# Kernel tuning notes

Measured on AMD Instinct MI355X. Metric: run time of the kernel, lower is better.

## Reference

```python
import jax, jax.numpy as jnp
import numpy as np

B, N, D_IN, D_HID, D_OUT = 4096, 64, 128, 128, 128


def setup_inputs() -> dict:
    key = jax.random.key(0)
    k1, k2, k3, k4, k5, k6 = jax.random.split(key, 6)
    inp = jax.random.normal(k1, (B, D_IN), dtype=jnp.float32)
    neigh = jax.random.normal(k2, (B, N, D_IN), dtype=jnp.float32)
    # zero out some neighbors so the mask path is exercised
    drop = jax.random.bernoulli(k3, 0.2, (B, N))
    neigh = jnp.where(drop[:, :, None], 0.0, neigh)
    W_mlp = jax.random.normal(k4, (D_HID, D_IN), dtype=jnp.float32) * (1.0 / np.sqrt(D_IN))
    b_mlp = jnp.zeros((D_HID,), dtype=jnp.float32)
    W_comb = jax.random.normal(k5, (2 * D_OUT, D_IN + D_HID), dtype=jnp.float32) * (1.0 / np.sqrt(D_IN + D_HID))
    b_comb = jax.random.normal(k6, (2 * D_OUT,), dtype=jnp.float32) * 0.01
    return {"input": inp, "neighbor_inputs": neigh, "W_mlp": W_mlp, "b_mlp": b_mlp,
            "W_comb": W_comb, "b_comb": b_comb}


def reference(input, neighbor_inputs, W_mlp, b_mlp, W_comb, b_comb):
    # mask: neighbors whose features sum to exactly 0 (padding)  [B, N, 1]
    mask = (jnp.sum(neighbor_inputs, axis=-1) == 0.0)[:, :, None]
    # per-neighbor MLP + ReLU: [B, N, D_HID]
    h = jax.nn.relu(jnp.einsum('bnd,hd->bnh', neighbor_inputs, W_mlp) + b_mlp)
    h = jnp.where(mask, 0.0, h)
    # max-pool over neighbor dim -> [B, D_HID]
    pooled = jnp.max(h, axis=1)
    # combine: concat + linear + ReLU -> [B, 2*D_OUT]
    combined = jnp.concatenate([input, pooled], axis=-1)
    out = jax.nn.relu(combined @ W_comb.T + b_comb)
    return out
```

## Files before the change

### kernel.cpp

```cpp
#include <hip/hip_runtime.h>
#include <hip/hip_bf16.h>

typedef __attribute__((ext_vector_type(4))) float f32x4;
typedef __attribute__((ext_vector_type(8))) short bf16x8;

#define N_NEI 64
#define D_IN  128
#define D_HID 128

union BF8 { bf16x8 v; __hip_bfloat162 h[4]; unsigned u[4]; };

__device__ __forceinline__ bf16x8 pack8(const float4& a, const float4& b) {
  BF8 r;
  r.h[0] = __float22bfloat162_rn(float2{a.x, a.y});
  r.h[1] = __float22bfloat162_rn(float2{a.z, a.w});
  r.h[2] = __float22bfloat162_rn(float2{b.x, b.y});
  r.h[3] = __float22bfloat162_rn(float2{b.z, b.w});
  return r.v;
}

__global__ __launch_bounds__(256, 4)
void k1_pool(const float* __restrict__ neigh, const float* __restrict__ Wmlp,
             const float* __restrict__ bmlp, unsigned short* __restrict__ pooled) {
  __shared__ unsigned short Wl[D_HID * D_IN];
  __shared__ float pscr[4][D_HID];

  const int tid = threadIdx.x;
  const int l = tid & 63;
  const int w = tid >> 6;
  const int lr = l & 15;
  const int lg = l >> 4;

  const int b = blockIdx.x * 4 + w;
  const float* rowbase = neigh + (size_t)b * N_NEI * D_IN;

  float4 pf[8];
  {
    const float* arow = rowbase + (size_t)lr * D_IN + lg * 8;
    #pragma unroll
    for (int ks = 0; ks < 4; ++ks) {
      pf[2 * ks]     = *(const float4*)(arow + ks * 32);
      pf[2 * ks + 1] = *(const float4*)(arow + ks * 32 + 4);
    }
  }

  const float4* W4 = (const float4*)Wmlp;
  #pragma unroll 4
  for (int it = 0; it < 8; ++it) {
    int f8 = it * 256 + tid;
    int j  = f8 >> 4;
    int d0 = (f8 & 15) * 8;
    float4 a = W4[f8 * 2];
    float4 bb = W4[f8 * 2 + 1];
    int byte = j * 256 + ((d0 * 2) ^ ((j & 7) << 4));
    *(bf16x8*)((char*)Wl + byte) = pack8(a, bb);
  }

  float bml[8];
  #pragma unroll
  for (int t = 0; t < 8; ++t) bml[t] = bmlp[t * 16 + lr];

  __syncthreads();

  float pmax[8];
  #pragma unroll
  for (int t = 0; t < 8; ++t) pmax[t] = 0.f;

  #pragma unroll 1
  for (int mt = 0; mt < 4; ++mt) {
    bf16x8 af[4];
    float rs = 0.f;
    #pragma unroll
    for (int ks = 0; ks < 4; ++ks) {
      float4 a0 = pf[2 * ks];
      float4 a1 = pf[2 * ks + 1];
      rs += a0.x + a0.y + a0.z + a0.w + a1.x + a1.y + a1.z + a1.w;
      af[ks] = pack8(a0, a1);
    }

    if (mt < 3) {
      const float* arow = rowbase + (size_t)((mt + 1) * 16 + lr) * D_IN + lg * 8;
      #pragma unroll
      for (int ks = 0; ks < 4; ++ks) {
        pf[2 * ks]     = *(const float4*)(arow + ks * 32);
        pf[2 * ks + 1] = *(const float4*)(arow + ks * 32 + 4);
      }
    }

    rs += __shfl_xor(rs, 16);
    rs += __shfl_xor(rs, 32);
    unsigned mask16 = (unsigned)(__ballot(rs == 0.0f) & 0xFFFFull);

    #pragma unroll 1
    for (int p = 0; p < 2; ++p) {
      f32x4 acc[4];
      #pragma unroll
      for (int tt = 0; tt < 4; ++tt) acc[tt] = (f32x4){0.f, 0.f, 0.f, 0.f};

      #pragma unroll
      for (int tt = 0; tt < 4; ++tt) {
        #pragma unroll
        for (int ks = 0; ks < 4; ++ks) {
          int jr = (p * 4 + tt) * 16 + lr;
          int d0 = ks * 32 + lg * 8;
          bf16x8 bf = *(const bf16x8*)((const char*)Wl + jr * 256 + ((d0 * 2) ^ ((jr & 7) << 4)));
          acc[tt] = __builtin_amdgcn_mfma_f32_16x16x32_bf16(af[ks], bf, acc[tt], 0, 0, 0);
        }
      }

      #pragma unroll
      for (int tt = 0; tt < 4; ++tt) {
        #pragma unroll
        for (int r = 0; r < 4; ++r) {
          int row = lg * 4 + r;
          float v = fmaxf(acc[tt][r] + bml[p * 4 + tt], 0.f);
          if ((mask16 >> row) & 1u) v = 0.f;
          pmax[p * 4 + tt] = fmaxf(pmax[p * 4 + tt], v);
        }
      }
    }
  }

  #pragma unroll
  for (int t = 0; t < 8; ++t) {
    pmax[t] = fmaxf(pmax[t], __shfl_xor(pmax[t], 16));
    pmax[t] = fmaxf(pmax[t], __shfl_xor(pmax[t], 32));
  }

  if (l < 16) {
    #pragma unroll
    for (int t = 0; t < 8; ++t) pscr[w][t * 16 + l] = pmax[t];
  }
  __syncthreads();
  float2 pv = *(const float2*)&pscr[w][2 * l];
  __hip_bfloat162 h2 = __float22bfloat162_rn(pv);
  ((unsigned*)(pooled + (size_t)b * D_HID))[l] = *(unsigned*)&h2;
}

__global__ __launch_bounds__(256, 2)
void k2_comb(const float* __restrict__ inp, const unsigned short* __restrict__ pooled,
             const float* __restrict__ Wcomb, const float* __restrict__ bcomb,
             float* __restrict__ out) {
  __shared__ unsigned short Wl[32 * 256];

  const int tid = threadIdx.x;
  const int l = tid & 63;
  const int w = tid >> 6;
  const int mchunk = blockIdx.x >> 3;
  const int c8     = blockIdx.x & 7;
  const int lr = l & 15;
  const int lg = l >> 4;

  const int row = mchunk * 64 + w * 16 + lr;

  float4 a0[4], a1[4];
  #pragma unroll
  for (int ks = 0; ks < 4; ++ks) {
    const float* p = inp + (size_t)row * 128 + ks * 32 + lg * 8;
    a0[ks] = *(const float4*)p;
    a1[ks] = *(const float4*)(p + 4);
  }
  bf16x8 af[8];
  #pragma unroll
  for (int ks = 4; ks < 8; ++ks) {
    af[ks] = *(const bf16x8*)(pooled + (size_t)row * 128 + (ks - 4) * 32 + lg * 8);
  }

  const float4* W4 = (const float4*)Wcomb;
  #pragma unroll
  for (int it = 0; it < 4; ++it) {
    int c  = it * 256 + tid;
    int jr = c >> 5;
    int d0 = (c & 31) * 8;
    int gidx = ((c8 * 32 + jr) * 256 + d0) >> 2;
    float4 a = W4[gidx];
    float4 bb = W4[gidx + 1];
    int byte = jr * 512 + ((d0 * 2) ^ ((jr & 7) << 4));
    *(bf16x8*)((char*)Wl + byte) = pack8(a, bb);
  }

  float bcl[2];
  #pragma unroll
  for (int t = 0; t < 2; ++t) bcl[t] = bcomb[c8 * 32 + t * 16 + lr];

  #pragma unroll
  for (int ks = 0; ks < 4; ++ks) af[ks] = pack8(a0[ks], a1[ks]);

  __syncthreads();

  f32x4 acc[2];
  #pragma unroll
  for (int t = 0; t < 2; ++t) acc[t] = (f32x4){0.f, 0.f, 0.f, 0.f};
  #pragma unroll
  for (int t = 0; t < 2; ++t) {
    #pragma unroll
    for (int ks = 0; ks < 8; ++ks) {
      int jr = t * 16 + lr;
      int d0 = ks * 32 + lg * 8;
      bf16x8 bf = *(const bf16x8*)((const char*)Wl + jr * 512 + ((d0 * 2) ^ ((jr & 7) << 4)));
      acc[t] = __builtin_amdgcn_mfma_f32_16x16x32_bf16(af[ks], bf, acc[t], 0, 0, 0);
    }
  }

  #pragma unroll
  for (int t = 0; t < 2; ++t) {
    #pragma unroll
    for (int r = 0; r < 4; ++r) {
      int ro = mchunk * 64 + w * 16 + lg * 4 + r;
      int co = c8 * 32 + t * 16 + lr;
      float v = acc[t][r] + bcl[t];
      out[(size_t)ro * 256 + co] = fmaxf(v, 0.f);
    }
  }
}

extern "C" void kernel_launch(void* const* d_in, const int* in_sizes, int n_in,
                              void* d_out, int out_size, void* d_ws, size_t ws_size,
                              hipStream_t stream) {
  const float* inp   = (const float*)d_in[0];
  const float* neigh = (const float*)d_in[1];
  const float* Wmlp  = (const float*)d_in[2];
  const float* bmlp  = (const float*)d_in[3];
  const float* Wcomb = (const float*)d_in[4];
  const float* bcomb = (const float*)d_in[5];
  float* out = (float*)d_out;
  unsigned short* pooled = (unsigned short*)d_ws;

  k1_pool<<<1024, 256, 0, stream>>>(neigh, Wmlp, bmlp, pooled);
  k2_comb<<<512, 256, 0, stream>>>(inp, pooled, Wcomb, bcomb, out);
}
```

Baseline: 42.92 us.

## Fuse neighbor max-pool and combine linear into a single kernel

```diff
diff --git a/kernel.cpp b/kernel.cpp
--- a/kernel.cpp
+++ b/kernel.cpp
@@ -19,11 +19,13 @@
   return r.v;
 }
 
-__global__ __launch_bounds__(256, 4)
-void k1_pool(const float* __restrict__ neigh, const float* __restrict__ Wmlp,
-             const float* __restrict__ bmlp, unsigned short* __restrict__ pooled) {
+__global__ __launch_bounds__(256, 2)
+void fused_pool_comb(const float* __restrict__ inp, const float* __restrict__ neigh,
+                     const float* __restrict__ Wmlp, const float* __restrict__ bmlp,
+                     const float* __restrict__ Wcomb, const float* __restrict__ bcomb,
+                     float* __restrict__ out) {
   __shared__ unsigned short Wl[D_HID * D_IN];
-  __shared__ float pscr[4][D_HID];
+  __shared__ float pscr[4][132];
 
   const int tid = threadIdx.x;
   const int l = tid & 63;
@@ -31,7 +33,8 @@
   const int lr = l & 15;
   const int lg = l >> 4;
 
-  const int b = blockIdx.x * 4 + w;
+  const int b0 = blockIdx.x * 4;
+  const int b = b0 + w;
   const float* rowbase = neigh + (size_t)b * N_NEI * D_IN;
 
   float4 pf[8];
@@ -45,7 +48,7 @@
   }
 
   const float4* W4 = (const float4*)Wmlp;
-  #pragma unroll 4
+  #pragma unroll
   for (int it = 0; it < 8; ++it) {
     int f8 = it * 256 + tid;
     int j  = f8 >> 4;
@@ -131,85 +134,46 @@
     #pragma unroll
     for (int t = 0; t < 8; ++t) pscr[w][t * 16 + l] = pmax[t];
   }
-  __syncthreads();
-  float2 pv = *(const float2*)&pscr[w][2 * l];
-  __hip_bfloat162 h2 = __float22bfloat162_rn(pv);
-  ((unsigned*)(pooled + (size_t)b * D_HID))[l] = *(unsigned*)&h2;
-}
 
-__global__ __launch_bounds__(256, 2)
-void k2_comb(const float* __restrict__ inp, const unsigned short* __restrict__ pooled,
-             const float* __restrict__ Wcomb, const float* __restrict__ bcomb,
-             float* __restrict__ out) {
-  __shared__ unsigned short Wl[32 * 256];
-
-  const int tid = threadIdx.x;
-  const int l = tid & 63;
-  const int w = tid >> 6;
-  const int mchunk = blockIdx.x >> 3;
-  const int c8     = blockIdx.x & 7;
-  const int lr = l & 15;
-  const int lg = l >> 4;
-
-  const int row = mchunk * 64 + w * 16 + lr;
-
-  float4 a0[4], a1[4];
-  #pragma unroll
-  for (int ks = 0; ks < 4; ++ks) {
-    const float* p = inp + (size_t)row * 128 + ks * 32 + lg * 8;
-    a0[ks] = *(const float4*)p;
-    a1[ks] = *(const float4*)(p + 4);
+  const int ar = b0 + (lr & 3);
+  bf16x8 caf[8];
+  {
+    const float* p = inp + (size_t)ar * D_IN + lg * 8;
+    #pragma unroll
+    for (int ks = 0; ks < 4; ++ks) {
+      float4 a0 = *(const float4*)(p + ks * 32);
+      float4 a1 = *(const float4*)(p + ks * 32 + 4);
+      caf[ks] = pack8(a0, a1);
+    }
   }
-  bf16x8 af[8];
-  #pragma unroll
-  for (int ks = 4; ks < 8; ++ks) {
-    af[ks] = *(const bf16x8*)(pooled + (size_t)row * 128 + (ks - 4) * 32 + lg * 8);
-  }
-
-  const float4* W4 = (const float4*)Wcomb;
-  #pragma unroll
-  for (int it = 0; it < 4; ++it) {
-    int c  = it * 256 + tid;
-    int jr = c >> 5;
-    int d0 = (c & 31) * 8;
-    int gidx = ((c8 * 32 + jr) * 256 + d0) >> 2;
-    float4 a = W4[gidx];
-    float4 bb = W4[gidx + 1];
-    int byte = jr * 512 + ((d0 * 2) ^ ((jr & 7) << 4));
-    *(bf16x8*)((char*)Wl + byte) = pack8(a, bb);
-  }
-
-  float bcl[2];
-  #pragma unroll
-  for (int t = 0; t < 2; ++t) bcl[t] = bcomb[c8 * 32 + t * 16 + lr];
-
-  #pragma unroll
-  for (int ks = 0; ks < 4; ++ks) af[ks] = pack8(a0[ks], a1[ks]);
 
   __syncthreads();
 
-  f32x4 acc[2];
   #pragma unroll
-  for (int t = 0; t < 2; ++t) acc[t] = (f32x4){0.f, 0.f, 0.f, 0.f};
-  #pragma unroll
-  for (int t = 0; t < 2; ++t) {
+  for (int ks = 0; ks < 4; ++ks) {
+    const float* p = &pscr[lr & 3][ks * 32 + lg * 8];
+    float4 a0 = *(const float4*)p;
+    float4 a1 = *(const float4*)(p + 4);
+    caf[4 + ks] = pack8(a0, a1);
+  }
+
+  #pragma unroll 1
+  for (int nt = 0; nt < 4; ++nt) {
+    const int jr = w * 64 + nt * 16 + lr;
+    const float* wp = Wcomb + (size_t)jr * 256;
+    f32x4 acc = (f32x4){0.f, 0.f, 0.f, 0.f};
     #pragma unroll
     for (int ks = 0; ks < 8; ++ks) {
-      int jr = t * 16 + lr;
-      int d0 = ks * 32 + lg * 8;
-      bf16x8 bf = *(const bf16x8*)((const char*)Wl + jr * 512 + ((d0 * 2) ^ ((jr & 7) << 4)));
-      acc[t] = __builtin_amdgcn_mfma_f32_16x16x32_bf16(af[ks], bf, acc[t], 0, 0, 0);
+      float4 w0 = *(const float4*)(wp + ks * 32 + lg * 8);
+      float4 w1 = *(const float4*)(wp + ks * 32 + lg * 8 + 4);
+      acc = __builtin_amdgcn_mfma_f32_16x16x32_bf16(caf[ks], pack8(w0, w1), acc, 0, 0, 0);
     }
-  }
-
-  #pragma unroll
-  for (int t = 0; t < 2; ++t) {
-    #pragma unroll
-    for (int r = 0; r < 4; ++r) {
-      int ro = mchunk * 64 + w * 16 + lg * 4 + r;
-      int co = c8 * 32 + t * 16 + lr;
-      float v = acc[t][r] + bcl[t];
-      out[(size_t)ro * 256 + co] = fmaxf(v, 0.f);
+    float bc = bcomb[jr];
+    if (lg == 0) {
+      #pragma unroll
+      for (int r = 0; r < 4; ++r) {
+        out[(size_t)(b0 + r) * 256 + jr] = fmaxf(acc[r] + bc, 0.f);
+      }
     }
   }
 }
@@ -224,8 +188,6 @@
   const float* Wcomb = (const float*)d_in[4];
   const float* bcomb = (const float*)d_in[5];
   float* out = (float*)d_out;
-  unsigned short* pooled = (unsigned short*)d_ws;
 
-  k1_pool<<<1024, 256, 0, stream>>>(neigh, Wmlp, bmlp, pooled);
-  k2_comb<<<512, 256, 0, stream>>>(inp, pooled, Wcomb, bcomb, out);
+  fused_pool_comb<<<1024, 256, 0, stream>>>(inp, neigh, Wmlp, bmlp, Wcomb, bcomb, out);
 }
```

Measured after the change: 58.26 us. 35.7% more time.
